# Performance work log

Measured on AMD Instinct MI355X. Metric: run time of the kernel, lower is better.

Reference implementation:

```python
import jax, jax.numpy as jnp
import numpy as np

DIM = 1024
H = 16
HKV = 4
HD = DIM // H  # 64
GROUP = H // HKV
ROPE_BASE = 10000.0
B, T = 2, 2048


def rms_norm(x, eps):
    return x * jax.lax.rsqrt(jnp.mean(x * x, axis=-1, keepdims=True) + eps)


def apply_rotary(x, cos, sin):
    # x: [B, h, T, HD]; cos/sin: [1, 1, T, HD//2]
    half = x.shape[-1] // 2
    x1, x2 = x[..., :half], x[..., half:]
    return jnp.concatenate([x1 * cos + x2 * sin, -x1 * sin + x2 * cos], axis=-1)


def setup_inputs() -> dict:
    key = jax.random.key(0)
    ks = jax.random.split(key, 5)
    s = 0.02
    return {
        "x": jax.random.normal(ks[0], (B, T, DIM), dtype=jnp.float32),
        "Wq": jax.random.normal(ks[1], (DIM, DIM), dtype=jnp.float32) * s,
        "Wk": jax.random.normal(ks[2], (HKV * HD, DIM), dtype=jnp.float32) * s,
        "Wv": jax.random.normal(ks[3], (HKV * HD, DIM), dtype=jnp.float32) * s,
        "Wproj": jax.random.normal(ks[4], (DIM, DIM), dtype=jnp.float32) * s,
        "q_gain": jnp.full((H,), 12.0, dtype=jnp.float32),
    }


def reference(x, Wq, Wk, Wv, Wproj, q_gain):
    bsz, seqlen, dim = x.shape
    eps = jnp.asarray(jnp.finfo(x.dtype).eps, x.dtype)

    # double RMSNorm path: normalized input for q/k, raw input for v
    x_qk = rms_norm(x, eps)
    q = (x_qk @ Wq.T).reshape(bsz, seqlen, H, HD).transpose(0, 2, 1, 3)    # [B,H,T,D]
    k = (x_qk @ Wk.T).reshape(bsz, seqlen, HKV, HD).transpose(0, 2, 1, 3)  # [B,Hkv,T,D]
    v = (x @ Wv.T).reshape(bsz, seqlen, HKV, HD).transpose(0, 2, 1, 3)     # [B,Hkv,T,D]

    q = rms_norm(q, eps)
    k = rms_norm(k, eps)

    # rotary embeddings
    t = jnp.arange(seqlen, dtype=jnp.float32)
    inv_freq = 1.0 / (ROPE_BASE ** (jnp.arange(0, HD, 2, dtype=jnp.float32) / HD))
    freqs = jnp.outer(t, inv_freq)                       # [T, HD//2]
    cos = jnp.cos(freqs)[None, None].astype(x.dtype)
    sin = jnp.sin(freqs)[None, None].astype(x.dtype)
    q = apply_rotary(q, cos, sin)
    k = apply_rotary(k, cos, sin)

    # per-head gain on q
    q = q * q_gain.astype(q.dtype)[None, :, None, None]

    # GQA: expand kv heads to query heads
    k_r = jnp.repeat(k, GROUP, axis=1)  # [B,H,T,D]
    v_r = jnp.repeat(v, GROUP, axis=1)

    scale = 1.0 / np.sqrt(HD)
    scores = jnp.einsum("bhqd,bhkd->bhqk", q, k_r) * scale
    causal = jnp.tril(jnp.ones((seqlen, seqlen), dtype=bool))
    scores = jnp.where(causal[None, None], scores, jnp.asarray(-jnp.inf, scores.dtype))
    attn = jax.nn.softmax(scores, axis=-1)
    y = jnp.einsum("bhqk,bhkd->bhqd", attn, v_r)          # [B,H,T,D]

    # XSA: remove value-direction component from output
    y_bt = y.transpose(0, 2, 1, 3)                        # [B,T,H,D]
    v_bt = v.transpose(0, 2, 1, 3)                        # [B,T,Hkv,D]
    y_g = y_bt.reshape(bsz, seqlen, HKV, GROUP, HD)
    vnorm = jnp.sqrt(jnp.sum(v_bt * v_bt, axis=-1, keepdims=True))
    vn = (v_bt / jnp.maximum(vnorm, 1e-12))[..., None, :]  # [B,T,Hkv,1,D]
    proj = jnp.sum(y_g * vn, axis=-1, keepdims=True) * vn
    y_bt = (y_g - proj).reshape(bsz, seqlen, H, HD)

    return y_bt.reshape(bsz, seqlen, dim) @ Wproj.T
```

## Files before the change

### kernel.cpp

```cpp
#include <hip/hip_runtime.h>
#include <hip/hip_bf16.h>

typedef __attribute__((ext_vector_type(8))) short bf8v;
typedef __attribute__((ext_vector_type(4))) float f4v;

#define MFMA16(a,b,c) __builtin_amdgcn_mfma_f32_16x16x32_bf16((a),(b),(c),0,0,0)

#define GLD16(gp, lp) __builtin_amdgcn_global_load_lds( \
    (const __attribute__((address_space(1))) void*)(gp), \
    (__attribute__((address_space(3))) void*)(lp), 16, 0, 0)

#define DIMC   1024
#define TSEQ   2048
#define NH     16
#define NKV    4
#define HDIM   64
#define RMS_EPS 1.1920929e-07f
#define QSCALE 0.1803368801111601f

__device__ __forceinline__ ushort f2bf(float f) {
  unsigned u = __builtin_bit_cast(unsigned, f);
  u = (u + 0x7FFFu + ((u >> 16) & 1u)) >> 16;
  return (ushort)u;
}
__device__ __forceinline__ float bf2f(ushort u) {
  return __builtin_bit_cast(float, (unsigned)u << 16);
}
__device__ __forceinline__ unsigned cvtpk(float lo, float hi) {
  unsigned r;
  asm("v_cvt_pk_bf16_f32 %0, %1, %2" : "=v"(r) : "v"(lo), "v"(hi));
  return r;
}

__global__ __launch_bounds__(256) void prep_all(
    const float* __restrict__ x,
    const float* __restrict__ Wq, const float* __restrict__ Wk,
    const float* __restrict__ Wv, const float* __restrict__ Wp,
    ushort* __restrict__ xhi, ushort* __restrict__ xlo,
    ushort* __restrict__ xb,
    ushort* __restrict__ wqkh, ushort* __restrict__ wqkl,
    ushort* __restrict__ wvb, ushort* __restrict__ wpb,
    float* __restrict__ cosT, float* __restrict__ sinT) {
  __shared__ float red[4];
  int bid = blockIdx.x, tid = threadIdx.x;
  if (bid < 4096) {
    int row = bid;
    int lane = tid & 63, w = tid >> 6;
    float4 v = ((const float4*)(x + (size_t)row * DIMC))[tid];
    float ss = v.x * v.x + v.y * v.y + v.z * v.z + v.w * v.w;
    for (int off = 32; off; off >>= 1) ss += __shfl_xor(ss, off);
    if (lane == 0) red[w] = ss;
    __syncthreads();
    float tot = red[0] + red[1] + red[2] + red[3];
    float rs = rsqrtf(tot * (1.0f / DIMC) + RMS_EPS);
    float n0 = v.x * rs, n1 = v.y * rs, n2 = v.z * rs, n3 = v.w * rs;
    ushort4 h, l, ob;
    h.x = f2bf(n0); l.x = f2bf(n0 - bf2f(h.x));
    h.y = f2bf(n1); l.y = f2bf(n1 - bf2f(h.y));
    h.z = f2bf(n2); l.z = f2bf(n2 - bf2f(h.z));
    h.w = f2bf(n3); l.w = f2bf(n3 - bf2f(h.w));
    ob.x = f2bf(v.x); ob.y = f2bf(v.y); ob.z = f2bf(v.z); ob.w = f2bf(v.w);
    ((ushort4*)(xhi + (size_t)row * DIMC))[tid] = h;
    ((ushort4*)(xlo + (size_t)row * DIMC))[tid] = l;
    ((ushort4*)(xb  + (size_t)row * DIMC))[tid] = ob;
    return;
  }
  int wb = bid - 4096;
  if (wb < 1280) {
    const float* src;
    size_t si, di;
    if (wb < 1024) { src = Wq; si = (size_t)wb * 256 + tid; di = si; }
    else { src = Wk; si = (size_t)(wb - 1024) * 256 + tid; di = 262144 + si; }
    float4 v = ((const float4*)src)[si];
    ushort4 h, l;
    h.x = f2bf(v.x); l.x = f2bf(v.x - bf2f(h.x));
    h.y = f2bf(v.y); l.y = f2bf(v.y - bf2f(h.y));
    h.z = f2bf(v.z); l.z = f2bf(v.z - bf2f(h.z));
    h.w = f2bf(v.w); l.w = f2bf(v.w - bf2f(h.w));
    ((ushort4*)wqkh)[di] = h;
    ((ushort4*)wqkl)[di] = l;
  } else if (wb < 2560) {
    const float* src;
    ushort* dst;
    int i;
    if (wb < 1536) { src = Wv; dst = wvb; i = (wb - 1280) * 256 + tid; }
    else           { src = Wp; dst = wpb; i = (wb - 1536) * 256 + tid; }
    float4 v = ((const float4*)src)[i];
    ushort4 o;
    o.x = f2bf(v.x); o.y = f2bf(v.y); o.z = f2bf(v.z); o.w = f2bf(v.w);
    ((ushort4*)dst)[i] = o;
  } else {
    int i = (wb - 2560) * 256 + tid;
    int t = i >> 5, j = i & 31;
    float inv = 1.0f / powf(10000.0f, (float)j * (1.0f / 32.0f));
    float f = (float)t * inv;
    cosT[i] = cosf(f);
    sinT[i] = sinf(f);
  }
}

__global__ __launch_bounds__(256, 3)
void gemm_qkv(const ushort* __restrict__ xhi, const ushort* __restrict__ xlo,
              const ushort* __restrict__ wqkh, const ushort* __restrict__ wqkl,
              float* __restrict__ QKf, ushort* __restrict__ QKc,
              const ushort* __restrict__ xb, const ushort* __restrict__ wvb,
              float* __restrict__ Vf) {
  __shared__ __align__(16) ushort lA[128 * 64];
  __shared__ __align__(16) ushort lB[128 * 64];
  const int bid = blockIdx.x;
  int u;
  bool big;
  if (bid < 256)      { big = true;  u = bid; }
  else if (bid < 448) { big = false; u = bid - 256; }
  else if (bid < 512) { big = true;  u = 256 + (bid - 448); }
  else                { big = false; u = 192 + (bid - 512); }

  const ushort *Ap0, *Bp0, *Ap1, *Bp1;
  float* Cf = QKf;
  int N = 1280, nsteps, mt, n0;
  if (big) {
    mt = u / 10; n0 = (u % 10) * 128;
    Ap0 = xlo; Bp0 = wqkh; Ap1 = xhi; Bp1 = wqkl; nsteps = 32;
  } else if (u < 320) {
    mt = u / 10; n0 = (u % 10) * 128;
    Ap0 = xhi; Bp0 = wqkh; Ap1 = Ap0; Bp1 = Bp0; nsteps = 16;
  } else {
    int v = u - 320; mt = v >> 1; n0 = (v & 1) * 128;
    Ap0 = xb; Bp0 = wvb; Ap1 = Ap0; Bp1 = Bp0; nsteps = 16;
    Cf = Vf; N = 256;
  }
  const int m0 = mt * 128;

  const int t = threadIdx.x;
  const int lane = t & 63, w = t >> 6;
  const int wr = w >> 1, wc = w & 1;
  const int l15 = lane & 15, lg = lane >> 4;
  const int srow = t >> 3, scp = t & 7;

  f4v acc[4][4] = {};

  for (int s = 0; s < nsteps; ++s) {
    const ushort* Ab = (s < 16) ? Ap0 : Ap1;
    const ushort* Bb = (s < 16) ? Bp0 : Bp1;
    const int kk = (s & 15) * 64;
    for (int i = 0; i < 4; ++i) {
      int row = srow + i * 32;
      int sc = scp ^ (row & 7);
      const ushort* ga = Ab + (size_t)(m0 + row) * DIMC + kk + sc * 8;
      const ushort* gb = Bb + (size_t)(n0 + row) * DIMC + kk + sc * 8;
      GLD16(ga, &lA[w * 512 + i * 2048]);
      GLD16(gb, &lB[w * 512 + i * 2048]);
    }
    __syncthreads();
    for (int kx = 0; kx < 2; ++kx) {
      bf8v af[4], bfr[4];
      for (int m = 0; m < 4; ++m) {
        int row = wr * 64 + m * 16 + l15;
        int ch = (kx * 4 + lg) ^ (row & 7);
        af[m] = *(const bf8v*)&lA[row * 64 + ch * 8];
      }
      for (int n = 0; n < 4; ++n) {
        int row = wc * 64 + n * 16 + l15;
        int ch = (kx * 4 + lg) ^ (row & 7);
        bfr[n] = *(const bf8v*)&lB[row * 64 + ch * 8];
      }
      for (int m = 0; m < 4; ++m)
        for (int n = 0; n < 4; ++n)
          acc[m][n] = MFMA16(af[m], bfr[n], acc[m][n]);
    }
    __syncthreads();
  }

  if (big) {
    for (int m = 0; m < 4; ++m)
      for (int n = 0; n < 4; ++n)
        for (int j = 0; j < 4; ++j) {
          int r = m0 + wr * 64 + m * 16 + lg * 4 + j;
          int c = n0 + wc * 64 + n * 16 + l15;
          QKc[(size_t)r * 1280 + c] = f2bf(acc[m][n][j]);
        }
  } else {
    for (int m = 0; m < 4; ++m)
      for (int n = 0; n < 4; ++n)
        for (int j = 0; j < 4; ++j) {
          int r = m0 + wr * 64 + m * 16 + lg * 4 + j;
          int c = n0 + wc * 64 + n * 16 + l15;
          Cf[(size_t)r * N + c] = acc[m][n][j];
        }
  }
}

__global__ __launch_bounds__(256, 2)
void gemm_bt(const ushort* __restrict__ A0, const ushort* __restrict__ B0,
             float* __restrict__ C, int N) {
  __shared__ __align__(16) ushort lA[128 * 64];
  __shared__ __align__(16) ushort lB[128 * 64];
  const int t = threadIdx.x;
  const int lane = t & 63, w = t >> 6;
  const int wr = w >> 1, wc = w & 1;
  const int l15 = lane & 15, lg = lane >> 4;
  const int m0 = blockIdx.y * 128, n0 = blockIdx.x * 128;
  const int srow = t >> 3, scp = t & 7;

  f4v acc[4][4] = {};

  for (int k0 = 0; k0 < 1024; k0 += 64) {
    for (int i = 0; i < 4; ++i) {
      int row = srow + i * 32;
      int sc = scp ^ (row & 7);
      const ushort* ga = A0 + (size_t)(m0 + row) * DIMC + k0 + sc * 8;
      const ushort* gb = B0 + (size_t)(n0 + row) * DIMC + k0 + sc * 8;
      GLD16(ga, &lA[w * 512 + i * 2048]);
      GLD16(gb, &lB[w * 512 + i * 2048]);
    }
    __syncthreads();
    for (int kx = 0; kx < 2; ++kx) {
      bf8v af[4], bfr[4];
      for (int m = 0; m < 4; ++m) {
        int row = wr * 64 + m * 16 + l15;
        int ch = (kx * 4 + lg) ^ (row & 7);
        af[m] = *(const bf8v*)&lA[row * 64 + ch * 8];
      }
      for (int n = 0; n < 4; ++n) {
        int row = wc * 64 + n * 16 + l15;
        int ch = (kx * 4 + lg) ^ (row & 7);
        bfr[n] = *(const bf8v*)&lB[row * 64 + ch * 8];
      }
      for (int m = 0; m < 4; ++m)
        for (int n = 0; n < 4; ++n)
          acc[m][n] = MFMA16(af[m], bfr[n], acc[m][n]);
    }
    __syncthreads();
  }

  for (int m = 0; m < 4; ++m)
    for (int n = 0; n < 4; ++n)
      for (int j = 0; j < 4; ++j) {
        int r = m0 + wr * 64 + m * 16 + lg * 4 + j;
        int c = n0 + wc * 64 + n * 16 + l15;
        C[(size_t)r * N + c] = acc[m][n][j];
      }
}

__global__ __launch_bounds__(256) void post_all(
    const float* __restrict__ QKf, const ushort* __restrict__ QKc,
    const float* __restrict__ cosT,
    const float* __restrict__ sinT, const float* __restrict__ qgain,
    ushort* __restrict__ qhi, ushort* __restrict__ qlo,
    ushort* __restrict__ kb16,
    const float* __restrict__ Vf, ushort* __restrict__ vt2,
    ushort* __restrict__ vhat_q) {
  __shared__ float lds[64][69];
  __shared__ float rnv[64];
  int bid = blockIdx.x;
  if (bid < 4096) {
    int m = bid;
    int b = m >> 11, tpos = m & 2047;
    int lane = threadIdx.x & 63, w = threadIdx.x >> 6;
    int d = lane, j = d & 31;
    float sgn = (d < 32) ? 1.0f : -1.0f;
    float c = cosT[tpos * 32 + j], s = sinT[tpos * 32 + j];

    for (int i = 0; i < 4; ++i) {
      int h = w * 4 + i;
      size_t base = (size_t)m * 1280 + h * HDIM + d;
      float q = QKf[base] + bf2f(QKc[base]);
      float ss = q * q;
      for (int off = 32; off; off >>= 1) ss += __shfl_xor(ss, off);
      float rs = rsqrtf(ss * (1.0f / HDIM) + RMS_EPS);
      float qn = q * rs;
      float partner = __shfl_xor(qn, 32);
      float ro = (qn * c + sgn * partner * s) * (qgain[h] * QSCALE);
      ushort hi = f2bf(ro);
      ushort lo = f2bf(ro - bf2f(hi));
      size_t idx = (((size_t)b * NH + h) * TSEQ + tpos) * HDIM + d;
      qhi[idx] = hi;
      qlo[idx] = lo;
    }
    {
      int kv = w;
      size_t base = (size_t)m * 1280 + 1024 + kv * HDIM + d;
      float k = QKf[base] + bf2f(QKc[base]);
      float ss = k * k;
      for (int off = 32; off; off >>= 1) ss += __shfl_xor(ss, off);
      float rs = rsqrtf(ss * (1.0f / HDIM) + RMS_EPS);
      float kn = k * rs;
      float partner = __shfl_xor(kn, 32);
      float ro = kn * c + sgn * partner * s;
      kb16[((size_t)(b * NKV + kv) * TSEQ + tpos) * HDIM + d] = f2bf(ro);
    }
    return;
  }
  {
    int vb = bid - 4096;
    int bkv = vb >> 5, tt = vb & 31;
    int b = bkv >> 2, kv = bkv & 3;
    int tid = threadIdx.x;
    for (int i = 0; i < 16; ++i) {
      int idx = i * 256 + tid;
      int tloc = idx >> 6, d = idx & 63;
      lds[d][tloc] = Vf[((size_t)(b * TSEQ + tt * 64 + tloc)) * 256 + kv * 64 + d];
    }
    __syncthreads();
    {
      int t = tid >> 2, prt = tid & 3;
      float ssum = 0.f;
      for (int dd = 0; dd < 16; ++dd) {
        float v = lds[prt * 16 + dd][t];
        ssum += v * v;
      }
      ssum += __shfl_xor(ssum, 1);
      ssum += __shfl_xor(ssum, 2);
      if (prt == 0) rnv[t] = 1.0f / fmaxf(sqrtf(ssum), 1e-12f);
    }
    __syncthreads();
    for (int i = 0; i < 16; ++i) {
      int idx = i * 256 + tid;
      int d = idx >> 6, tloc = idx & 63;
      vt2[(size_t)bkv * (TSEQ * 64) + tt * 4096 + d * 64 + tloc] = f2bf(lds[d][tloc]);
    }
    for (int i = 0; i < 16; ++i) {
      int idx = i * 256 + tid;
      int tloc = idx >> 6, d = idx & 63;
      vhat_q[((size_t)bkv * TSEQ + tt * 64 + tloc) * 64 + d] =
          f2bf(lds[d][tloc] * rnv[tloc]);
    }
  }
}

__global__ __launch_bounds__(256, 4) void attn_chunk(
    const ushort* __restrict__ qhi, const ushort* __restrict__ qlo,
    const ushort* __restrict__ kb16, const ushort* __restrict__ vt2,
    ushort* __restrict__ pyb, float* __restrict__ pml) {
  __shared__ __align__(16) ushort lk[2][64 * 64];
  __shared__ __align__(16) ushort lv[2][64 * 64];
  __shared__ __align__(16) unsigned pl[4][512];
  const int t = threadIdx.x;
  const int lane = t & 63, w = t >> 6;
  const int bid = blockIdx.x;
  const int combo = bid & 31;
  const int s = 59 - (bid >> 5);
  int tile, ci;
  if (s < 12)      { tile = s; ci = 0; }
  else if (s < 36) { tile = 12 + ((s - 12) >> 1); ci = (s - 12) & 1; }
  else             { int z = s - 36; tile = 24 + z / 3; ci = z % 3; }
  const int nch = (tile <= 11) ? 1 : (tile <= 23 ? 2 : 3);
  const int ktot = tile + 1, base = ktot / nch, rem = ktot % nch;
  const int kb0 = ci * base + (ci < rem ? ci : rem);
  const int len = base + (ci < rem ? 1 : 0);

  const int xcd = combo & 7, g = (combo >> 3) & 3;
  const int b = xcd >> 2, kv = xcd & 3, h = kv * 4 + g;
  const int l15 = lane & 15, lg = lane >> 4;
  const int q0 = tile * 64 + w * 16;
  const int t3 = t >> 3, tc8 = t & 7;
  const int rx = l15 & 7;
  const int pswz = rx << 2;

  const size_t qoff = (((size_t)(b * NH + h)) * TSEQ + q0 + l15) * HDIM;
  bf8v bq0h = *(const bf8v*)(qhi + qoff + lg * 8);
  bf8v bq1h = *(const bf8v*)(qhi + qoff + 32 + lg * 8);
  bf8v bq0l = *(const bf8v*)(qlo + qoff + lg * 8);
  bf8v bq1l = *(const bf8v*)(qlo + qoff + 32 + lg * 8);

  const ushort* kb = kb16 + (size_t)(b * NKV + kv) * TSEQ * 64;
  const ushort* vb = vt2 + (size_t)(b * NKV + kv) * TSEQ * 64;
  unsigned* pw = &pl[w][0];

#define STAGE(BUF, KT) do { \
    _Pragma("unroll") \
    for (int i = 0; i < 2; ++i) { \
      int row = i * 32 + t3; \
      int sc = tc8 ^ (row & 7); \
      GLD16(kb + (size_t)((KT) * 64 + row) * 64 + sc * 8, \
            &lk[BUF][(i * 32 + (w << 3)) * 64]); \
      GLD16(vb + (size_t)(KT) * 4096 + row * 64 + sc * 8, \
            &lv[BUF][(i * 32 + (w << 3)) * 64]); \
    } } while (0)

  STAGE(0, kb0);

  f4v y[4] = {};
  float mrow = -1e30f, lrow = 0.f;

#pragma unroll 1
  for (int itc = 0; itc < len; ++itc) {
    const int cur = itc & 1;
    const int kt = kb0 + itc;
    __syncthreads();
    if (itc + 1 < len) STAGE(cur ^ 1, kt + 1);

    const ushort* lkc = &lk[cur][0];
    const ushort* lvc = &lv[cur][0];
    const int kv0 = kt * 64;

    f4v s4[4];
    __builtin_amdgcn_s_setprio(1);
#pragma unroll
    for (int n = 0; n < 4; ++n) {
      const ushort* krow = lkc + (n * 16 + l15) * 64;
      bf8v kh0 = *(const bf8v*)&krow[((0 + lg) ^ rx) * 8];
      bf8v kh1 = *(const bf8v*)&krow[((4 + lg) ^ rx) * 8];
      f4v z = {};
      f4v acc = MFMA16(kh0, bq0h, z);
      acc = MFMA16(kh1, bq1h, acc);
      acc = MFMA16(kh0, bq0l, acc);
      acc = MFMA16(kh1, bq1l, acc);
      s4[n] = acc;
    }
    __builtin_amdgcn_s_setprio(0);

    const bool need_mask = (kt == tile);
    float mloc = -1e30f;
#pragma unroll
    for (int n = 0; n < 4; ++n)
#pragma unroll
      for (int j = 0; j < 4; ++j) {
        float v = s4[n][j];
        if (need_mask && (kv0 + n * 16 + lg * 4 + j > q0 + l15)) v = -1e30f;
        s4[n][j] = v;
        mloc = fmaxf(mloc, v);
      }
    if (__any(mloc > mrow + 11.5f)) {
      float mf = fmaxf(mloc, __shfl_xor(mloc, 16));
      mf = fmaxf(mf, __shfl_xor(mf, 32));
      float mnew = fmaxf(mrow, mf);
      float scf = exp2f(mrow - mnew);
      lrow *= scf;
#pragma unroll
      for (int n = 0; n < 4; ++n) y[n] *= scf;
      mrow = mnew;
    }
#pragma unroll
    for (int n = 0; n < 4; ++n)
#pragma unroll
      for (int j = 0; j < 4; ++j) {
        float e = exp2f(s4[n][j] - mrow);
        s4[n][j] = e;
        lrow += e;
      }

#pragma unroll
    for (int n = 0; n < 4; ++n) {
      uint2 pk;
      pk.x = cvtpk(s4[n][0], s4[n][1]);
      pk.y = cvtpk(s4[n][2], s4[n][3]);
      *(uint2*)&pw[l15 * 32 + ((8 * n + 2 * lg) ^ pswz)] = pk;
    }
    asm volatile("s_waitcnt lgkmcnt(0)" ::: "memory");
    bf8v pb0 = *(const bf8v*)&pw[l15 * 32 + ((lg * 4) ^ pswz)];
    bf8v pb1 = *(const bf8v*)&pw[l15 * 32 + ((16 + lg * 4) ^ pswz)];
    __builtin_amdgcn_s_setprio(1);
#pragma unroll
    for (int n = 0; n < 4; ++n) {
      const ushort* vrow = lvc + (n * 16 + l15) * 64;
      bf8v va0 = *(const bf8v*)&vrow[((0 + lg) ^ rx) * 8];
      bf8v va1 = *(const bf8v*)&vrow[((4 + lg) ^ rx) * 8];
      y[n] = MFMA16(va0, pb0, y[n]);
      y[n] = MFMA16(va1, pb1, y[n]);
    }
    __builtin_amdgcn_s_setprio(0);
  }
#undef STAGE

  {
    lrow += __shfl_xor(lrow, 16);
    lrow += __shfl_xor(lrow, 32);
    const int slot = combo * 60 + s;
    ushort* pb = pyb + (size_t)slot * 4096;
    const int q = w * 16 + l15;
#pragma unroll
    for (int n = 0; n < 4; ++n) {
      uint2 pk;
      pk.x = cvtpk(y[n][0], y[n][1]);
      pk.y = cvtpk(y[n][2], y[n][3]);
      *(uint2*)&pb[q * 64 + n * 16 + lg * 4] = pk;
    }
    if (lane < 16) {
      float* mlp = pml + (size_t)slot * 128;
      mlp[q] = mrow;
      mlp[64 + q] = lrow;
    }
  }
}

__global__ __launch_bounds__(256) void combine_kern(
    const ushort* __restrict__ pyb, const float* __restrict__ pml,
    const ushort* __restrict__ vhat_q, ushort* __restrict__ ytil) {
  const int bid = blockIdx.x;
  const int combo = bid & 31, tile = bid >> 5;
  const int xcd = combo & 7, g = (combo >> 3) & 3;
  const int b = xcd >> 2, kv = xcd & 3, h = kv * 4 + g;
  const int nch = (tile <= 11) ? 1 : (tile <= 23 ? 2 : 3);
  const int sb = (tile <= 11) ? tile
               : (tile <= 23) ? 12 + 2 * (tile - 12)
                              : 36 + 3 * (tile - 24);
  const int tid = threadIdx.x;
  const int q = tid >> 2, ds = (tid & 3) * 16;
  const int q0 = tile * 64;

  float m[3], l[3];
#pragma unroll
  for (int ci = 0; ci < 3; ++ci) {
    if (ci < nch) {
      const float* mlp = pml + (size_t)(combo * 60 + sb + ci) * 128;
      m[ci] = mlp[q];
      l[ci] = mlp[64 + q];
    } else { m[ci] = -1e30f; l[ci] = 0.f; }
  }
  float M = fmaxf(m[0], fmaxf(m[1], m[2]));
  float y[16] = {};
  float ltot = 0.f;
#pragma unroll
  for (int ci = 0; ci < 3; ++ci) {
    if (ci < nch) {
      float sc = exp2f(m[ci] - M);
      ltot += l[ci] * sc;
      const ushort* pb = pyb + (size_t)(combo * 60 + sb + ci) * 4096 + q * 64 + ds;
      bf8v p0 = *(const bf8v*)pb;
      bf8v p1 = *(const bf8v*)(pb + 8);
#pragma unroll
      for (int dd = 0; dd < 8; ++dd) {
        y[dd] += sc * bf2f((ushort)p0[dd]);
        y[8 + dd] += sc * bf2f((ushort)p1[dd]);
      }
    }
  }
  float inv = 1.0f / ltot;
  const ushort* vh = vhat_q + ((size_t)(b * NKV + kv) * TSEQ + q0 + q) * 64 + ds;
  bf8v v0 = *(const bf8v*)vh;
  bf8v v1 = *(const bf8v*)(vh + 8);
  float vv[16];
  float dp = 0.f;
#pragma unroll
  for (int dd = 0; dd < 8; ++dd) {
    vv[dd] = bf2f((ushort)v0[dd]);
    vv[8 + dd] = bf2f((ushort)v1[dd]);
  }
#pragma unroll
  for (int dd = 0; dd < 16; ++dd) {
    y[dd] *= inv;
    dp += y[dd] * vv[dd];
  }
  dp += __shfl_xor(dp, 1);
  dp += __shfl_xor(dp, 2);
  bf8v o0, o1;
#pragma unroll
  for (int dd = 0; dd < 8; ++dd) {
    o0[dd] = (short)f2bf(y[dd] - dp * vv[dd]);
    o1[dd] = (short)f2bf(y[8 + dd] - dp * vv[8 + dd]);
  }
  ushort* yo = ytil + ((size_t)(b * TSEQ + q0 + q)) * DIMC + h * HDIM + ds;
  *(bf8v*)yo = o0;
  *(bf8v*)(yo + 8) = o1;
}

extern "C" void kernel_launch(void* const* d_in, const int* in_sizes, int n_in,
                              void* d_out, int out_size, void* d_ws, size_t ws_size,
                              hipStream_t stream) {
  (void)in_sizes; (void)n_in; (void)out_size; (void)ws_size;
  const float* x  = (const float*)d_in[0];
  const float* Wq = (const float*)d_in[1];
  const float* Wk = (const float*)d_in[2];
  const float* Wv = (const float*)d_in[3];
  const float* Wp = (const float*)d_in[4];
  const float* qg = (const float*)d_in[5];
  float* out = (float*)d_out;
  char* ws = (char*)d_ws;
  const size_t KB = 1024, MB = 1ull << 20;

  ushort* xhi = (ushort*)(ws);
  ushort* xlo = (ushort*)(ws + 8 * MB);
  ushort* xb  = (ushort*)(ws + 16 * MB);
  ushort* wqkh = (ushort*)(ws + 24 * MB);
  ushort* wqkl = (ushort*)(ws + 26 * MB + 512 * KB);
  ushort* wvb = (ushort*)(ws + 29 * MB);
  ushort* wpb = (ushort*)(ws + 29 * MB + 512 * KB);
  float*  cosT = (float*)(ws + 31 * MB + 512 * KB);
  float*  sinT = (float*)(ws + 31 * MB + 768 * KB);
  float*  QKf  = (float*)(ws + 32 * MB);
  ushort* kb16 = (ushort*)(ws + 52 * MB);
  ushort* vt2  = (ushort*)(ws + 54 * MB);

  float*  Vf   = out;
  ushort* QKc  = (ushort*)((char*)out + 4 * MB);
  ushort* vhat_q = (ushort*)((char*)out + 14 * MB);
  ushort* qhb  = xhi;
  ushort* qlb  = xlo;
  ushort* ytil = xb;
  ushort* pyb = (ushort*)(ws + 32 * MB);
  float*  pml = (float*)(ws + 48 * MB);

  prep_all<<<6912, 256, 0, stream>>>(x, Wq, Wk, Wv, Wp, xhi, xlo, xb,
                                     wqkh, wqkl, wvb, wpb, cosT, sinT);

  gemm_qkv<<<704, 256, 0, stream>>>(xhi, xlo, wqkh, wqkl, QKf, QKc,
                                    xb, wvb, Vf);

  post_all<<<4352, 256, 0, stream>>>(QKf, QKc, cosT, sinT, qg, qhb, qlb, kb16,
                                     Vf, vt2, vhat_q);
  attn_chunk<<<1920, 256, 0, stream>>>(qhb, qlb, kb16, vt2, pyb, pml);
  combine_kern<<<1024, 256, 0, stream>>>(pyb, pml, vhat_q, ytil);
  gemm_bt<<<dim3(8, 32), 256, 0, stream>>>(ytil, wpb, out, 1024);
}
```

Measured before the change: 146.5 us.

## Rebalance attention split-K chunks via LUT schedule and reuse K buffer for P

The attention kernel's work split changes: instead of 1-3 chunks per query tile, it uses up to 4 chunks of at most 8 KV tiles each. A static lookup table orders the 80 work items longest-first to reduce the tail imbalance, and the combine kernel and launch sizes are updated to match. The per-wave P staging buffer now lives inside the current K LDS buffer, guarded by an extra barrier. This frees LDS so the launch bound can rise to 5 blocks per SM, in exchange for one more barrier per iteration and more partial results to combine.

```diff
diff --git a/kernel.cpp b/kernel.cpp
--- a/kernel.cpp
+++ b/kernel.cpp
@@ -328,26 +328,50 @@
   }
 }
 
-__global__ __launch_bounds__(256, 4) void attn_chunk(
+#define E(s,t,k,l) ((unsigned)(s) | ((unsigned)(t) << 8) | \
+                    ((unsigned)(k) << 16) | ((unsigned)(l) << 24))
+__global__ __launch_bounds__(256, 5) void attn_chunk(
     const ushort* __restrict__ qhi, const ushort* __restrict__ qlo,
     const ushort* __restrict__ kb16, const ushort* __restrict__ vt2,
     ushort* __restrict__ pyb, float* __restrict__ pml) {
+  static const unsigned LUT[80] = {
+    E(76,31,0,8), E(77,31,8,8), E(78,31,16,8), E(79,31,24,8),
+    E(72,30,0,8), E(73,30,8,8), E(74,30,16,8),
+    E(68,29,0,8), E(69,29,8,8), E(64,28,0,8),
+    E(45,23,0,8), E(46,23,8,8), E(47,23,16,8),
+    E(42,22,0,8), E(43,22,8,8), E(39,21,0,8),
+    E(22,15,0,8), E(23,15,8,8), E(20,14,0,8), E(7,7,0,8),
+    E(75,30,24,7), E(70,29,16,7), E(71,29,23,7),
+    E(65,28,8,7), E(66,28,15,7), E(67,28,22,7),
+    E(60,27,0,7), E(61,27,7,7), E(62,27,14,7), E(63,27,21,7),
+    E(56,26,0,7), E(57,26,7,7), E(58,26,14,7),
+    E(52,25,0,7), E(53,25,7,7), E(48,24,0,7),
+    E(44,22,16,7), E(40,21,8,7), E(41,21,15,7),
+    E(36,20,0,7), E(37,20,7,7), E(38,20,14,7),
+    E(33,19,0,7), E(34,19,7,7), E(30,18,0,7),
+    E(21,14,8,7), E(18,13,0,7), E(19,13,7,7), E(16,12,0,7), E(6,6,0,7),
+    E(59,26,21,6), E(54,25,14,6), E(55,25,20,6),
+    E(49,24,7,6), E(50,24,13,6), E(51,24,19,6),
+    E(35,19,14,6), E(31,18,7,6), E(32,18,13,6),
+    E(27,17,0,6), E(28,17,6,6), E(29,17,12,6),
+    E(24,16,0,6), E(25,16,6,6),
+    E(17,12,7,6), E(14,11,0,6), E(15,11,6,6), E(12,10,0,6), E(5,5,0,6),
+    E(26,16,12,5), E(13,10,6,5), E(10,9,0,5), E(11,9,5,5),
+    E(8,8,0,5), E(4,4,0,5),
+    E(9,8,5,4), E(3,3,0,4),
+    E(2,2,0,3), E(1,1,0,2), E(0,0,0,1)
+  };
   __shared__ __align__(16) ushort lk[2][64 * 64];
   __shared__ __align__(16) ushort lv[2][64 * 64];
-  __shared__ __align__(16) unsigned pl[4][512];
   const int t = threadIdx.x;
   const int lane = t & 63, w = t >> 6;
   const int bid = blockIdx.x;
   const int combo = bid & 31;
-  const int s = 59 - (bid >> 5);
-  int tile, ci;
-  if (s < 12)      { tile = s; ci = 0; }
-  else if (s < 36) { tile = 12 + ((s - 12) >> 1); ci = (s - 12) & 1; }
-  else             { int z = s - 36; tile = 24 + z / 3; ci = z % 3; }
-  const int nch = (tile <= 11) ? 1 : (tile <= 23 ? 2 : 3);
-  const int ktot = tile + 1, base = ktot / nch, rem = ktot % nch;
-  const int kb0 = ci * base + (ci < rem ? ci : rem);
-  const int len = base + (ci < rem ? 1 : 0);
+  const unsigned e = LUT[bid >> 5];
+  const int slot = e & 255;
+  const int tile = (e >> 8) & 31;
+  const int kb0 = (e >> 16) & 31;
+  const int len = (int)(e >> 24);
 
   const int xcd = combo & 7, g = (combo >> 3) & 3;
   const int b = xcd >> 2, kv = xcd & 3, h = kv * 4 + g;
@@ -365,7 +389,6 @@
 
   const ushort* kb = kb16 + (size_t)(b * NKV + kv) * TSEQ * 64;
   const ushort* vb = vt2 + (size_t)(b * NKV + kv) * TSEQ * 64;
-  unsigned* pw = &pl[w][0];
 
 #define STAGE(BUF, KT) do { \
     _Pragma("unroll") \
@@ -392,6 +415,7 @@
 
     const ushort* lkc = &lk[cur][0];
     const ushort* lvc = &lv[cur][0];
+    unsigned* pw = (unsigned*)&lk[cur][w << 10];
     const int kv0 = kt * 64;
 
     f4v s4[4];
@@ -435,10 +459,13 @@
     for (int n = 0; n < 4; ++n)
 #pragma unroll
       for (int j = 0; j < 4; ++j) {
-        float e = exp2f(s4[n][j] - mrow);
-        s4[n][j] = e;
-        lrow += e;
-      }
+        float e2 = exp2f(s4[n][j] - mrow);
+        s4[n][j] = e2;
+        lrow += e2;
+      }
+
+    asm volatile("s_waitcnt lgkmcnt(0)" ::: "memory");
+    __builtin_amdgcn_s_barrier();
 
 #pragma unroll
     for (int n = 0; n < 4; ++n) {
@@ -466,8 +493,8 @@
   {
     lrow += __shfl_xor(lrow, 16);
     lrow += __shfl_xor(lrow, 32);
-    const int slot = combo * 60 + s;
-    ushort* pb = pyb + (size_t)slot * 4096;
+    const int pslot = combo * 80 + slot;
+    ushort* pb = pyb + (size_t)pslot * 4096;
     const int q = w * 16 + l15;
 #pragma unroll
     for (int n = 0; n < 4; ++n) {
@@ -477,12 +504,13 @@
       *(uint2*)&pb[q * 64 + n * 16 + lg * 4] = pk;
     }
     if (lane < 16) {
-      float* mlp = pml + (size_t)slot * 128;
+      float* mlp = pml + (size_t)pslot * 128;
       mlp[q] = mrow;
       mlp[64 + q] = lrow;
     }
   }
 }
+#undef E
 
 __global__ __launch_bounds__(256) void combine_kern(
     const ushort* __restrict__ pyb, const float* __restrict__ pml,
@@ -491,32 +519,33 @@
   const int combo = bid & 31, tile = bid >> 5;
   const int xcd = combo & 7, g = (combo >> 3) & 3;
   const int b = xcd >> 2, kv = xcd & 3, h = kv * 4 + g;
-  const int nch = (tile <= 11) ? 1 : (tile <= 23 ? 2 : 3);
-  const int sb = (tile <= 11) ? tile
-               : (tile <= 23) ? 12 + 2 * (tile - 12)
-                              : 36 + 3 * (tile - 24);
+  const int nch = (tile + 8) >> 3;
+  const int sb = (tile < 8) ? tile
+               : (tile < 16) ? 8 + ((tile - 8) << 1)
+               : (tile < 24) ? 24 + 3 * (tile - 16)
+                             : 48 + ((tile - 24) << 2);
   const int tid = threadIdx.x;
   const int q = tid >> 2, ds = (tid & 3) * 16;
   const int q0 = tile * 64;
 
-  float m[3], l[3];
-#pragma unroll
-  for (int ci = 0; ci < 3; ++ci) {
+  float m[4], l[4];
+#pragma unroll
+  for (int ci = 0; ci < 4; ++ci) {
     if (ci < nch) {
-      const float* mlp = pml + (size_t)(combo * 60 + sb + ci) * 128;
+      const float* mlp = pml + (size_t)(combo * 80 + sb + ci) * 128;
       m[ci] = mlp[q];
       l[ci] = mlp[64 + q];
     } else { m[ci] = -1e30f; l[ci] = 0.f; }
   }
-  float M = fmaxf(m[0], fmaxf(m[1], m[2]));
+  float M = fmaxf(fmaxf(m[0], m[1]), fmaxf(m[2], m[3]));
   float y[16] = {};
   float ltot = 0.f;
 #pragma unroll
-  for (int ci = 0; ci < 3; ++ci) {
+  for (int ci = 0; ci < 4; ++ci) {
     if (ci < nch) {
       float sc = exp2f(m[ci] - M);
       ltot += l[ci] * sc;
-      const ushort* pb = pyb + (size_t)(combo * 60 + sb + ci) * 4096 + q * 64 + ds;
+      const ushort* pb = pyb + (size_t)(combo * 80 + sb + ci) * 4096 + q * 64 + ds;
       bf8v p0 = *(const bf8v*)pb;
       bf8v p1 = *(const bf8v*)(pb + 8);
 #pragma unroll
@@ -589,7 +618,7 @@
   ushort* qlb  = xlo;
   ushort* ytil = xb;
   ushort* pyb = (ushort*)(ws + 32 * MB);
-  float*  pml = (float*)(ws + 48 * MB);
+  float*  pml = (float*)(ws + 56 * MB);
 
   prep_all<<<6912, 256, 0, stream>>>(x, Wq, Wk, Wv, Wp, xhi, xlo, xb,
                                      wqkh, wqkl, wvb, wpb, cosT, sinT);
@@ -599,7 +628,7 @@
 
   post_all<<<4352, 256, 0, stream>>>(QKf, QKc, cosT, sinT, qg, qhb, qlb, kb16,
                                      Vf, vt2, vhat_q);
-  attn_chunk<<<1920, 256, 0, stream>>>(qhb, qlb, kb16, vt2, pyb, pml);
+  attn_chunk<<<2560, 256, 0, stream>>>(qhb, qlb, kb16, vt2, pyb, pml);
   combine_kern<<<1024, 256, 0, stream>>>(pyb, pml, vhat_q, ytil);
   gemm_bt<<<dim3(8, 32), 256, 0, stream>>>(ytil, wpb, out, 1024);
 }
```

Result: no change. 144.7 us (-1.2%).
